# Performance work log

Measured on AMD Instinct MI355X. Metric: run time of the kernel, lower is better.

The kernel has to match this reference:

```python
import jax, jax.numpy as jnp
import numpy as np

B, P, K, KS = 512, 64, 30, 4      # graphs, nodes per graph, sort-pool k, conv1d kernel
N, E, F, H = B * P, 524288, 128, 256
N_CLASSES = 10
L_OUT = K - KS + 1                 # 27, conv1d output length


def _sage(h, wl, wr, b, src, dst, inv_deg):
    # PyG SAGEConv (mean aggr): out = lin_l(mean_j x_j) + lin_r(x_i); bias only on lin_l
    agg = jax.ops.segment_sum(h[src], dst, num_segments=N) * inv_deg
    return jax.nn.relu(agg @ wl + b + h @ wr)


def setup_inputs() -> dict:
    key = jax.random.key(0)
    ks = jax.random.split(key, 32)
    x = jax.random.normal(ks[0], (N, F), jnp.float32)
    # intra-graph random edges (src -> dst aggregation)
    g = jax.random.randint(ks[1], (E,), 0, B)
    src = g * P + jax.random.randint(ks[2], (E,), 0, P)
    dst = g * P + jax.random.randint(ks[3], (E,), 0, P)
    edge_index = jnp.stack([src, dst]).astype(jnp.int32)
    batch = jnp.repeat(jnp.arange(B), P).astype(jnp.int32)  # sorted graph ids

    def lin(k, i, o):
        return jax.random.normal(k, (i, o), jnp.float32) / np.float32(np.sqrt(i))

    inp = {"x": x, "edge_index": edge_index, "batch": batch}
    dims = [(F, H), (H, H), (H, H), (H, H)]
    ki = 4
    for li, (i, o) in enumerate(dims):
        inp[f"sage{li}_wl"] = lin(ks[ki], i, o); ki += 1
        inp[f"sage{li}_wr"] = lin(ks[ki], i, o); ki += 1
        inp[f"sage{li}_b"] = jnp.zeros((o,), jnp.float32)
    inp["conv1d_w"] = jax.random.normal(ks[ki], (H, H, KS), jnp.float32) / np.float32(np.sqrt(H * KS)); ki += 1
    inp["conv1d_b"] = jnp.zeros((H,), jnp.float32)
    inp["lin1_w"] = lin(ks[ki], H * L_OUT, H); ki += 1
    inp["lin1_b"] = jnp.zeros((H,), jnp.float32)
    inp["lin2_w"] = lin(ks[ki], H, 128); ki += 1
    inp["lin2_b"] = jnp.zeros((128,), jnp.float32)
    inp["out_w"] = lin(ks[ki], 128, N_CLASSES); ki += 1
    inp["out_b"] = jnp.zeros((N_CLASSES,), jnp.float32)
    return inp


def reference(x, edge_index, batch,
              sage0_wl, sage0_wr, sage0_b,
              sage1_wl, sage1_wr, sage1_b,
              sage2_wl, sage2_wr, sage2_b,
              sage3_wl, sage3_wr, sage3_b,
              conv1d_w, conv1d_b, lin1_w, lin1_b,
              lin2_w, lin2_b, out_w, out_b):
    src, dst = edge_index[0], edge_index[1]
    deg = jax.ops.segment_sum(jnp.ones(src.shape, x.dtype), dst, num_segments=N)
    inv_deg = (1.0 / jnp.maximum(deg, 1.0))[:, None]

    h = jnp.nan_to_num(x, nan=0.0)
    h = _sage(h, sage0_wl, sage0_wr, sage0_b, src, dst, inv_deg)
    h = _sage(h, sage1_wl, sage1_wr, sage1_b, src, dst, inv_deg)
    h = _sage(h, sage2_wl, sage2_wr, sage2_b, src, dst, inv_deg)
    h = _sage(h, sage3_wl, sage3_wr, sage3_b, src, dst, inv_deg)  # [N, H]

    # SortAggregation(k=K): to dense batch, sort by last channel desc, top-k, zero-pad
    counts = jax.ops.segment_sum(jnp.ones(N, jnp.int32), batch, num_segments=B)
    offsets = jnp.cumsum(counts) - counts
    pos = jnp.arange(N) - offsets[batch]
    D = h.shape[1]
    dense = jnp.zeros((B, P, D), h.dtype).at[batch, pos].set(h)
    valid = jnp.zeros((B, P), bool).at[batch, pos].set(True)
    skey = jnp.where(valid, dense[..., -1], -jnp.inf)
    order = jnp.argsort(-skey, axis=1)[:, :K]                       # [B, K]
    topk = jnp.take_along_axis(dense, order[..., None], axis=1)     # [B, K, D]
    tvalid = jnp.take_along_axis(valid, order, axis=1)
    topk = jnp.where(tvalid[..., None], topk, 0.0)

    # x.view(B, K, -1).permute(0, 2, 1) -> [B, D, K]
    xc = topk.transpose(0, 2, 1)
    y = jax.lax.conv_general_dilated(xc, conv1d_w, (1,), 'VALID',
                                     dimension_numbers=('NCH', 'OIH', 'NCH'))
    y = jax.nn.relu(y + conv1d_b[None, :, None])                    # [B, H, L_OUT]
    y = y.reshape(B, -1)                                            # dropout is identity in eval
    y = jax.nn.relu(y @ lin1_w + lin1_b)
    y = jax.nn.relu(y @ lin2_w + lin2_b)
    return jax.nn.relu(y @ out_w + out_b)                           # [B, N_CLASSES]
```

## Files before the change

kernel.cpp:

```cpp
#include <hip/hip_runtime.h>
#include <hip/hip_bf16.h>

#define NNODES 32768
#define NEDGES 524288
#define NGRAPH 512
#define PNODES 64
#define KTOP 30
#define FIN 128
#define HID 256
#define LOUT 27

#define C1F 4.8828125e-4f
#define C2F 2.384185791015625e-7f

using f16x8 = __attribute__((ext_vector_type(8))) _Float16;
using f16x4 = __attribute__((ext_vector_type(4))) _Float16;
using f32x4 = __attribute__((ext_vector_type(4))) float;
using f32x16 = __attribute__((ext_vector_type(16))) float;
using u32x4 = __attribute__((ext_vector_type(4))) uint32_t;

template<int N> struct IC { static constexpr int v = N; };

#define GLDS(src, dst) __builtin_amdgcn_global_load_lds( \
    (const __attribute__((address_space(1))) void*)(src), \
    (__attribute__((address_space(3))) void*)(dst), 16, 0, 0)

__global__ void hist_kernel(const int* __restrict__ dst, int* __restrict__ counts) {
    int e = blockIdx.x * blockDim.x + threadIdx.x;
    if (e < NEDGES) atomicAdd(&counts[dst[e]], 1);
}

__global__ __launch_bounds__(1024) void scan_block_kernel(const int* __restrict__ counts,
        int* __restrict__ loc, int* __restrict__ partial) {
    int b = blockIdx.x, t = threadIdx.x;
    int i = b * 1024 + t;
    int v = counts[i];
    int lane = t & 63, w = t >> 6;
    int x = v;
    #pragma unroll
    for (int d = 1; d < 64; d <<= 1) { int y = __shfl_up(x, d, 64); if (lane >= d) x += y; }
    __shared__ int ws[16];
    if (lane == 63) ws[w] = x;
    __syncthreads();
    if (w == 0) {
        int s = (lane < 16) ? ws[lane] : 0;
        #pragma unroll
        for (int d = 1; d < 16; d <<= 1) { int y = __shfl_up(s, d, 64); if (lane >= d) s += y; }
        if (lane < 16) ws[lane] = s;
    }
    __syncthreads();
    int base = (w > 0) ? ws[w - 1] : 0;
    int incl = base + x;
    loc[i] = incl - v;
    if (t == 1023) partial[b] = incl;
}

__global__ __launch_bounds__(1024) void scan_fixup_kernel(const int* __restrict__ loc,
        const int* __restrict__ partial, const int* __restrict__ counts,
        int* __restrict__ offsets, int* __restrict__ cursor, float* __restrict__ invdeg) {
    int b = blockIdx.x, t = threadIdx.x;
    int i = b * 1024 + t;
    __shared__ int sbase;
    if (t == 0) { int s = 0; for (int j = 0; j < b; ++j) s += partial[j]; sbase = s; }
    __syncthreads();
    int o = loc[i] + sbase;
    offsets[i] = o;
    cursor[i] = o;
    invdeg[i] = 1.0f / fmaxf((float)counts[i], 1.0f);
}

__global__ void scatter_kernel(const int* __restrict__ src, const int* __restrict__ dst,
        int* __restrict__ cursor, int* __restrict__ ssrc) {
    int e = blockIdx.x * blockDim.x + threadIdx.x;
    if (e < NEDGES) {
        int d = dst[e];
        int p = atomicAdd(&cursor[d], 1);
        ssrc[p] = ((d & 63) << 6) | (src[e] & 63);
    }
}

__global__ void nan2num_split_kernel(const float* __restrict__ x,
        _Float16* __restrict__ oh, _Float16* __restrict__ ol, int n4) {
    int i = blockIdx.x * blockDim.x + threadIdx.x;
    if (i >= n4) return;
    float4 v = *(const float4*)(x + i * 4);
    float xs[4] = {v.x, v.y, v.z, v.w};
    f16x4 hh, ll;
    #pragma unroll
    for (int q = 0; q < 4; ++q) {
        float a = xs[q];
        a = (a != a) ? 0.f : a;
        _Float16 h = (_Float16)a;
        hh[q] = h;
        ll[q] = (_Float16)((a - (float)h) * 2048.0f);
    }
    *(f16x4*)(oh + (size_t)i * 4) = hh;
    *(f16x4*)(ol + (size_t)i * 4) = ll;
}

struct PrepSage {
    const float* src[8];
    _Float16* dh[8];
    _Float16* dl[8];
    int logK[8];
    int part[8];
};

__global__ __launch_bounds__(256) void prep_sage_kernel(PrepSage p) {
    int y = blockIdx.y;
    int idx = blockIdx.x * 256 + threadIdx.x;
    int lk = p.logK[y], K = 1 << lk;
    if (idx >= 256 * K) return;
    int n = idx >> lk, k = idx & (K - 1);
    float w = p.src[y][(size_t)k * 256 + n];
    _Float16 h = (_Float16)w;
    int wv = n >> 5, l31 = n & 31;
    int c = k >> 5, h2 = (k >> 4) & 1, hb = (k >> 3) & 1, j = k & 7;
    int NCH = K >> 5;
    size_t dst = (size_t)(wv * 2 + p.part[y]) * (size_t)(NCH * 1024)
               + (size_t)(c * 2 + h2) * 512 + (size_t)(hb * 32 + l31) * 8 + j;
    p.dh[y][dst] = h;
    p.dl[y][dst] = (_Float16)((w - (float)h) * 2048.0f);
}

__global__ __launch_bounds__(256) void prep_conv_kernel(const float* __restrict__ W,
        _Float16* __restrict__ b0, _Float16* __restrict__ b1) {
    int idx = blockIdx.x * 256 + threadIdx.x;
    int o = idx >> 10, k = idx & 1023;
    float w = W[(size_t)o * 1024 + (k & 255) * 4 + (k >> 8)];
    _Float16 h = (_Float16)w;
    b0[(size_t)o * 1024 + k] = h;
    b1[(size_t)o * 1024 + k] = (_Float16)((w - (float)h) * 2048.0f);
}

__global__ __launch_bounds__(256) void prep_lin1_kernel(const float* __restrict__ l1w,
        _Float16* __restrict__ wh, _Float16* __restrict__ wl_) {
    __shared__ float sh[64][65];
    int kb = blockIdx.x * 64;
    int nb = blockIdx.y * 64;
    int t = threadIdx.x;
    {
        int kk = t >> 2;
        int nc = (t & 3) * 16;
        int k = kb + kk, l = k >> 8, c = k & 255;
        const float* srow = l1w + (size_t)(c * 27 + l) * 256 + nb + nc;
        #pragma unroll
        for (int j = 0; j < 16; j += 4) {
            float4 v = *(const float4*)(srow + j);
            sh[kk][nc + j + 0] = v.x;
            sh[kk][nc + j + 1] = v.y;
            sh[kk][nc + j + 2] = v.z;
            sh[kk][nc + j + 3] = v.w;
        }
    }
    __syncthreads();
    {
        int nn = t >> 2;
        int kc = (t & 3) * 16;
        f16x8 oh[2], ol[2];
        #pragma unroll
        for (int j = 0; j < 16; ++j) {
            float x = sh[kc + j][nn];
            _Float16 h = (_Float16)x;
            oh[j >> 3][j & 7] = h;
            ol[j >> 3][j & 7] = (_Float16)((x - (float)h) * 2048.0f);
        }
        size_t o = (size_t)(nb + nn) * 6912 + kb + kc;
        *(f16x8*)(wh + o) = oh[0];
        *(f16x8*)(wh + o + 8) = oh[1];
        *(f16x8*)(wl_ + o) = ol[0];
        *(f16x8*)(wl_ + o + 8) = ol[1];
    }
}

struct SageWAll {
    const _Float16* wh[4];
    const _Float16* wl[4];
    const float* bias[4];
};

__global__ __launch_bounds__(512, 2) void fused_sage_all_kernel(
        const _Float16* __restrict__ hh, const _Float16* __restrict__ hl,
        const int* __restrict__ offsets, const int* __restrict__ counts,
        const int* __restrict__ ssrc, const float* __restrict__ invdeg,
        SageWAll W,
        _Float16* __restrict__ outh, _Float16* __restrict__ outl) {
    __shared__ __align__(16) _Float16 hp[2][8 * 2048];
    __shared__ __align__(16) uint32_t Sw[4096];
    const int g = blockIdx.x, t = threadIdx.x;
    const int lane = t & 63, wave = t >> 6;
    const int l31 = lane & 31, hb = lane >> 5;

    #pragma unroll
    for (int i = 0; i < 8; ++i) Sw[t + i * 512] = 0;

    {
        int a = lane >> 2, b = lane & 3;
        #pragma unroll
        for (int u0 = 0; u0 < 4; ++u0) {
            int u = u0 * 8 + wave;
            int part = u & 1;
            int cs = u >> 1;
            int c = cs >> 2, stripe = cs & 3;
            int row = stripe * 16 + a;
            int o = b ^ ((row >> 1) & 3) ^ (c & 3);
            const _Float16* src = (part ? hl : hh) + (size_t)g * (64 * FIN)
                                + (size_t)row * FIN + c * 32 + o * 8;
            GLDS(src, &hp[part][c * 2048 + stripe * 512]);
        }
    }
    const int gbeg = offsets[g * 64];
    const int gend = offsets[g * 64 + 63] + counts[g * 64 + 63];
    __syncthreads();

    for (int e = gbeg + t; e < gend; e += 512)
        atomicAdd(&Sw[ssrc[e] & 4095], 1u);
    __syncthreads();

    {
        int d = t >> 3, o = t & 7;
        float idg = invdeg[g * 64 + d];
        float v[8];
        #pragma unroll
        for (int j = 0; j < 8; ++j) v[j] = (float)Sw[(d << 6) + (o << 3) + j] * idg;
        __syncthreads();
        _Float16* Sp = (_Float16*)Sw;
        f16x8 s0, s1;
        #pragma unroll
        for (int j = 0; j < 8; ++j) {
            _Float16 h1 = (_Float16)v[j];
            s0[j] = h1;
            s1[j] = (_Float16)((v[j] - (float)h1) * 2048.0f);
        }
        int addr = (d << 6) + ((o ^ (d & 7)) << 3);
        *(f16x8*)&Sp[addr] = s0;
        *(f16x8*)&Sp[4096 + addr] = s1;
    }
    __syncthreads();

    const int col = (wave << 5) + l31;

    auto gemmKV = [&](auto NC, const _Float16* __restrict__ Bh,
                      const _Float16* __restrict__ Bl,
                      f32x16& a00, f32x16& a01, f32x16& a10, f32x16& a11) {
        constexpr int NCH = decltype(NC)::v;
        #pragma unroll 2
        for (int c = 0; c < NCH; ++c) {
            #pragma unroll
            for (int h2 = 0; h2 < 2; ++h2) {
                int slot = (2 * h2 + hb) ^ ((l31 >> 1) & 3) ^ (c & 3);
                int addr = c * 2048 + (l31 << 5) + (slot << 3);
                f16x8 ah0 = *(const f16x8*)&hp[0][addr];
                f16x8 al0 = *(const f16x8*)&hp[1][addr];
                f16x8 ah1 = *(const f16x8*)&hp[0][addr + 1024];
                f16x8 al1 = *(const f16x8*)&hp[1][addr + 1024];
                int ko = ((c << 1) + h2) * 512 + (lane << 3);
                f16x8 bh = *(const f16x8*)(Bh + ko);
                f16x8 bl = *(const f16x8*)(Bl + ko);
                a00 = __builtin_amdgcn_mfma_f32_32x32x16_f16(ah0, bh, a00, 0, 0, 0);
                a10 = __builtin_amdgcn_mfma_f32_32x32x16_f16(al0, bh, a10, 0, 0, 0);
                a10 = __builtin_amdgcn_mfma_f32_32x32x16_f16(ah0, bl, a10, 0, 0, 0);
                a01 = __builtin_amdgcn_mfma_f32_32x32x16_f16(ah1, bh, a01, 0, 0, 0);
                a11 = __builtin_amdgcn_mfma_f32_32x32x16_f16(al1, bh, a11, 0, 0, 0);
                a11 = __builtin_amdgcn_mfma_f32_32x32x16_f16(ah1, bl, a11, 0, 0, 0);
            }
        }
    };

    auto packpair = [](float x, float y, uint32_t& hw, uint32_t& lw) {
        _Float16 xh = (_Float16)x, yh = (_Float16)y;
        _Float16 xl = (_Float16)((x - (float)xh) * 2048.0f);
        _Float16 yl = (_Float16)((y - (float)yh) * 2048.0f);
        hw = (uint32_t)__builtin_bit_cast(unsigned short, xh)
           | ((uint32_t)__builtin_bit_cast(unsigned short, yh) << 16);
        lw = (uint32_t)__builtin_bit_cast(unsigned short, xl)
           | ((uint32_t)__builtin_bit_cast(unsigned short, yl) << 16);
    };

    auto spass = [&](int soffBase, const f32x16& pf0, const f32x16& pf1, f32x16& qf) {
        const _Float16* Sp = (const _Float16*)Sw;
        f32x16 sA = 0.f, sB = 0.f;
        #pragma unroll
        for (int kc = 0; kc < 4; ++kc) {
            const f32x16& pfk = (kc < 2) ? pf0 : pf1;
            const int i0 = ((2 * kc) & 3) * 4, i1 = ((2 * kc + 1) & 3) * 4;
            float kv0 = hb ? pfk[i1 + 0] : pfk[i0 + 0];
            float kv1 = hb ? pfk[i1 + 1] : pfk[i0 + 1];
            float kv2 = hb ? pfk[i1 + 2] : pfk[i0 + 2];
            float kv3 = hb ? pfk[i1 + 3] : pfk[i0 + 3];
            float sv0 = hb ? pfk[i0 + 0] : pfk[i1 + 0];
            float sv1 = hb ? pfk[i0 + 1] : pfk[i1 + 1];
            float sv2 = hb ? pfk[i0 + 2] : pfk[i1 + 2];
            float sv3 = hb ? pfk[i0 + 3] : pfk[i1 + 3];
            uint32_t kh0, kl0, kh1, kl1, sh0, sl0, sh1, sl1;
            packpair(kv0, kv1, kh0, kl0);
            packpair(kv2, kv3, kh1, kl1);
            packpair(sv0, sv1, sh0, sl0);
            packpair(sv2, sv3, sh1, sl1);
            uint32_t rh0 = (uint32_t)__shfl_xor((int)sh0, 32, 64);
            uint32_t rh1 = (uint32_t)__shfl_xor((int)sh1, 32, 64);
            uint32_t rl0 = (uint32_t)__shfl_xor((int)sl0, 32, 64);
            uint32_t rl1 = (uint32_t)__shfl_xor((int)sl1, 32, 64);
            u32x4 bhu, blu;
            bhu[0] = hb ? rh0 : kh0;  bhu[1] = hb ? rh1 : kh1;
            bhu[2] = hb ? kh0 : rh0;  bhu[3] = hb ? kh1 : rh1;
            blu[0] = hb ? rl0 : kl0;  blu[1] = hb ? rl1 : kl1;
            blu[2] = hb ? kl0 : rl0;  blu[3] = hb ? kl1 : rl1;
            f16x8 bhv = __builtin_bit_cast(f16x8, bhu);
            f16x8 blv = __builtin_bit_cast(f16x8, blu);
            int soff = soffBase + (l31 << 6) + (((2 * kc + hb) ^ (l31 & 7)) << 3);
            f16x8 s0a = *(const f16x8*)&Sp[soff];
            f16x8 s1a = *(const f16x8*)&Sp[4096 + soff];
            sA = __builtin_amdgcn_mfma_f32_32x32x16_f16(s0a, bhv, sA, 0, 0, 0);
            sB = __builtin_amdgcn_mfma_f32_32x32x16_f16(s0a, blv, sB, 0, 0, 0);
            sB = __builtin_amdgcn_mfma_f32_32x32x16_f16(s1a, bhv, sB, 0, 0, 0);
        }
        qf += sA + C1F * sB;
    };

    auto run_layer = [&](auto NC, const _Float16* __restrict__ Wsh,
                         const _Float16* __restrict__ Wsl,
                         const float* __restrict__ bias,
                         f32x16& sC0, f32x16& sC1) {
        constexpr size_t wstride = (size_t)decltype(NC)::v * 1024;
        f32x16 q00 = 0.f, q01 = 0.f, q10 = 0.f, q11 = 0.f;
        gemmKV(NC, Wsh + (size_t)((wave << 1) + 1) * wstride,
               Wsl + (size_t)((wave << 1) + 1) * wstride, q00, q01, q10, q11);
        f32x16 qf0 = q00 + C1F * q10;
        f32x16 qf1 = q01 + C1F * q11;

        f32x16 p00 = 0.f, p01 = 0.f, p10 = 0.f, p11 = 0.f;
        gemmKV(NC, Wsh + (size_t)(wave << 1) * wstride,
               Wsl + (size_t)(wave << 1) * wstride, p00, p01, p10, p11);
        f32x16 pf0 = p00 + C1F * p10;
        f32x16 pf1 = p01 + C1F * p11;

        spass(0, pf0, pf1, qf0);
        spass(2048, pf0, pf1, qf1);

        const float bb = bias[col];
        #pragma unroll
        for (int reg = 0; reg < 16; ++reg) {
            sC0[reg] = fmaxf(qf0[reg] + bb, 0.f);
            sC1[reg] = fmaxf(qf1[reg] + bb, 0.f);
        }
    };

    auto hp_write = [&](const f32x16& sC0, const f32x16& sC1) {
        int oc = l31 >> 3, j = l31 & 7;
        #pragma unroll
        for (int mi = 0; mi < 2; ++mi)
            #pragma unroll
            for (int reg = 0; reg < 16; ++reg) {
                int row = (mi << 5) + (reg & 3) + ((reg >> 2) << 3) + (hb << 2);
                int slot = oc ^ ((row >> 1) & 3) ^ (wave & 3);
                int addr = wave * 2048 + (row << 5) + (slot << 3) + j;
                float v = mi ? sC1[reg] : sC0[reg];
                _Float16 h1 = (_Float16)v;
                hp[0][addr] = h1;
                hp[1][addr] = (_Float16)((v - (float)h1) * 2048.0f);
            }
    };

    f32x16 sC0, sC1;
    run_layer(IC<4>{}, W.wh[0], W.wl[0], W.bias[0], sC0, sC1);
    __syncthreads();
    hp_write(sC0, sC1);
    __syncthreads();
    run_layer(IC<8>{}, W.wh[1], W.wl[1], W.bias[1], sC0, sC1);
    __syncthreads();
    hp_write(sC0, sC1);
    __syncthreads();
    run_layer(IC<8>{}, W.wh[2], W.wl[2], W.bias[2], sC0, sC1);
    __syncthreads();
    hp_write(sC0, sC1);
    __syncthreads();
    run_layer(IC<8>{}, W.wh[3], W.wl[3], W.bias[3], sC0, sC1);
    __syncthreads();
    _Float16* eL = &hp[0][0];
    #pragma unroll
    for (int part = 0; part < 2; ++part) {
        #pragma unroll
        for (int mi = 0; mi < 2; ++mi) {
            #pragma unroll
            for (int reg = 0; reg < 16; ++reg) {
                int row = (mi << 5) + (reg & 3) + ((reg >> 2) << 3) + (hb << 2);
                int cx = col ^ ((((row >> 2) & 1) << 5) | ((row & 3) << 3));
                float v = mi ? sC1[reg] : sC0[reg];
                _Float16 h1 = (_Float16)v;
                eL[(row << 8) + cx] = part ? (_Float16)((v - (float)h1) * 2048.0f) : h1;
            }
        }
        __syncthreads();
        _Float16* gout = part ? outl : outh;
        #pragma unroll
        for (int it = 0; it < 4; ++it) {
            int i = (t << 3) + (it << 12);
            int row = i >> 8, cc = i & 255;
            int sx = cc ^ ((((row >> 2) & 1) << 5) | ((row & 3) << 3));
            f16x8 v8 = *(const f16x8*)&eL[(row << 8) + sx];
            *(f16x8*)(gout + (size_t)((g << 6) + row) * HID + cc) = v8;
        }
        if (part == 0) __syncthreads();
    }
}

template<int NPROD, int CONV, int NPAIRS, int EPI>
__global__ __launch_bounds__(256, 2) void mfma_ps_kernel(
        const _Float16* __restrict__ A1h, const _Float16* __restrict__ A1l,
        const _Float16* __restrict__ A2h, const _Float16* __restrict__ A2l,
        const _Float16* __restrict__ B1h, const _Float16* __restrict__ B1l,
        const _Float16* __restrict__ B2h, const _Float16* __restrict__ B2l,
        const float* __restrict__ bias,
        _Float16* __restrict__ outh, _Float16* __restrict__ outl,
        float* __restrict__ Cpart,
        int lda, int K, int Nd, int nrb) {
    __shared__ _Float16 As[2][2][128 * 32];
    __shared__ _Float16 Bs[2][2][128 * 32];
    const int t = threadIdx.x;
    const int lane = t & 63, wave = t >> 6;
    const int wr = wave & 1, wc = wave >> 1;
    const int bid = blockIdx.x;
    const int rb = bid % nrb, cb = bid / nrb;
    const int row0 = rb * 128, col0 = cb * 128;
    const int l31 = lane & 31, hb = lane >> 5, x3 = l31 & 3;
    const int r16 = lane >> 2;
    const int qsrc8 = ((lane & 3) ^ (r16 & 3)) * 8;
    size_t aoffj[2], boffj[2];
    #pragma unroll
    for (int j = 0; j < 2; ++j) {
        int ar = row0 + wave * 32 + j * 16 + r16;
        aoffj[j] = CONV ? ((size_t)ar * 256 + (size_t)(ar / 27) * 768)
                        : (size_t)ar * (size_t)lda;
        boffj[j] = (size_t)(col0 + wave * 32 + j * 16 + r16) * (size_t)K;
    }
    int aroff[2], broff[2], slot8[2];
    #pragma unroll
    for (int mi = 0; mi < 2; ++mi) aroff[mi] = (wr * 64 + mi * 32 + l31) * 32;
    #pragma unroll
    for (int ni = 0; ni < 2; ++ni) broff[ni] = (wc * 64 + ni * 32 + l31) * 32;
    #pragma unroll
    for (int h = 0; h < 2; ++h) slot8[h] = ((2 * h + hb) ^ x3) * 8;

    const int KV = NPAIRS * K;
    const int kchunk = KV / gridDim.z;
    const int kv_lo = blockIdx.z * kchunk, kv_hi = kv_lo + kchunk;

    f32x16 acc0[2][2], acc1[2][2], acc2[2][2];
    #pragma unroll
    for (int i = 0; i < 2; ++i)
        #pragma unroll
        for (int j = 0; j < 2; ++j) { acc0[i][j] = 0.f; acc1[i][j] = 0.f; acc2[i][j] = 0.f; }

    auto stage = [&](int kv, int b) {
        int p = (NPAIRS == 2 && kv >= K) ? 1 : 0;
        int k = kv - p * K;
        const _Float16* __restrict__ sAh = p ? A2h : A1h;
        const _Float16* __restrict__ sAl = p ? A2l : A1l;
        const _Float16* __restrict__ sBh = p ? B2h : B1h;
        const _Float16* __restrict__ sBl = p ? B2l : B1l;
        #pragma unroll
        for (int j = 0; j < 2; ++j) {
            int ldsbase = (wave * 32 + j * 16) * 32;
            size_t ga = aoffj[j] + k + qsrc8;
            size_t gb = boffj[j] + k + qsrc8;
            GLDS(sAh + ga, &As[b][0][ldsbase]);
            GLDS(sAl + ga, &As[b][1][ldsbase]);
            GLDS(sBh + gb, &Bs[b][0][ldsbase]);
            GLDS(sBl + gb, &Bs[b][1][ldsbase]);
        }
    };

    stage(kv_lo, 0);
    __syncthreads();
    int b = 0;
    for (int kv = kv_lo; kv < kv_hi; kv += 32) {
        if (kv + 32 < kv_hi) stage(kv + 32, b ^ 1);
        #pragma unroll
        for (int h = 0; h < 2; ++h) {
            f16x8 af0[2], af1[2], bf0[2], bf1[2];
            #pragma unroll
            for (int mi = 0; mi < 2; ++mi) {
                af0[mi] = *(const f16x8*)&As[b][0][aroff[mi] + slot8[h]];
                af1[mi] = *(const f16x8*)&As[b][1][aroff[mi] + slot8[h]];
            }
            #pragma unroll
            for (int ni = 0; ni < 2; ++ni) {
                bf0[ni] = *(const f16x8*)&Bs[b][0][broff[ni] + slot8[h]];
                bf1[ni] = *(const f16x8*)&Bs[b][1][broff[ni] + slot8[h]];
            }
            #pragma unroll
            for (int mi = 0; mi < 2; ++mi)
                #pragma unroll
                for (int ni = 0; ni < 2; ++ni) {
                    acc0[mi][ni] = __builtin_amdgcn_mfma_f32_32x32x16_f16(af0[mi], bf0[ni], acc0[mi][ni], 0, 0, 0);
                    acc1[mi][ni] = __builtin_amdgcn_mfma_f32_32x32x16_f16(af1[mi], bf0[ni], acc1[mi][ni], 0, 0, 0);
                    acc1[mi][ni] = __builtin_amdgcn_mfma_f32_32x32x16_f16(af0[mi], bf1[ni], acc1[mi][ni], 0, 0, 0);
                    if (NPROD == 4)
                        acc2[mi][ni] = __builtin_amdgcn_mfma_f32_32x32x16_f16(af1[mi], bf1[ni], acc2[mi][ni], 0, 0, 0);
                }
        }
        b ^= 1;
        __syncthreads();
    }

    const int rquad = 4 * hb;
    #pragma unroll
    for (int ni = 0; ni < 2; ++ni) {
        int col = col0 + wc * 64 + ni * 32 + l31;
        float bb = (EPI == 0) ? bias[col] : 0.f;
        #pragma unroll
        for (int mi = 0; mi < 2; ++mi) {
            #pragma unroll
            for (int reg = 0; reg < 16; ++reg) {
                float v = acc0[mi][ni][reg] + C1F * acc1[mi][ni][reg];
                if (NPROD == 4) v += C2F * acc2[mi][ni][reg];
                int row = row0 + wr * 64 + mi * 32 + (reg & 3) + 8 * (reg >> 2) + rquad;
                if (EPI == 0) {
                    v = fmaxf(v + bb, 0.f);
                    _Float16 h = (_Float16)v;
                    size_t o = (size_t)row * Nd + col;
                    outh[o] = h;
                    outl[o] = (_Float16)((v - (float)h) * 2048.0f);
                } else {
                    size_t zb = (size_t)blockIdx.z * (size_t)(nrb * 128) * Nd;
                    Cpart[zb + (size_t)row * Nd + col] = v;
                }
            }
        }
    }
}

__global__ __launch_bounds__(256) void sortgather_kernel(const _Float16* __restrict__ hh,
        const _Float16* __restrict__ hl, _Float16* __restrict__ th, _Float16* __restrict__ tl) {
    __shared__ float vals[PNODES];
    __shared__ int ord[KTOP];
    int g = blockIdx.x, t = threadIdx.x;
    if (t < PNODES) {
        size_t idx = (size_t)(g * PNODES + t) * HID + (HID - 1);
        vals[t] = (float)hh[idx] + C1F * (float)hl[idx];
    }
    __syncthreads();
    if (t < PNODES) {
        float v = vals[t];
        int rank = 0;
        for (int j = 0; j < PNODES; ++j) {
            float vj = vals[j];
            rank += (vj > v) || (vj == v && j < t);
        }
        if (rank < KTOP) ord[rank] = g * PNODES + t;
    }
    __syncthreads();
    int c8 = (t & 31) * 8;
    for (int r = t >> 5; r < KTOP; r += 8) {
        size_t s = (size_t)ord[r] * HID + c8;
        size_t d = (size_t)(g * KTOP + r) * HID + c8;
        *(f16x8*)(th + d) = *(const f16x8*)(hh + s);
        *(f16x8*)(tl + d) = *(const f16x8*)(hl + s);
    }
}

__global__ void reduce_conv_kernel(const float* __restrict__ yb32,
        const float* __restrict__ b, _Float16* __restrict__ ybh, _Float16* __restrict__ ybl) {
    int i = blockIdx.x * 256 + threadIdx.x;
    float v = fmaxf(yb32[i] + yb32[i + 13824 * 256] + b[i & 255], 0.f);
    _Float16 h = (_Float16)v;
    ybh[i] = h;
    ybl[i] = (_Float16)((v - (float)h) * 2048.0f);
}

__global__ void reduce_lin1_kernel(const float* __restrict__ z1p,
        const float* __restrict__ b, float* __restrict__ z1) {
    int i = blockIdx.x * 256 + threadIdx.x;
    float s = b[i & 255];
    #pragma unroll
    for (int z = 0; z < 27; ++z) s += z1p[(size_t)z * 131072 + i];
    z1[i] = fmaxf(s, 0.f);
}

__global__ __launch_bounds__(256) void gemm64_kernel(
        const float* __restrict__ A, const float* __restrict__ B,
        const float* __restrict__ bias, float* __restrict__ C,
        int lda, int kend, int Nd) {
    __shared__ float As[16][64];
    __shared__ float Bs[16][64];
    const int tid = threadIdx.x;
    const int tx = tid & 15, ty = tid >> 4;
    const int la_r = tid >> 2, la_c = (tid & 3) << 2;
    const int lb_r = tid >> 4, lb_c = (tid & 15) << 2;
    const int row0 = blockIdx.x * 64, col0 = blockIdx.y * 64;
    const size_t aoff = (size_t)(row0 + la_r) * (size_t)lda;
    float acc[4][4] = {};
    for (int k0 = 0; k0 < kend; k0 += 16) {
        __syncthreads();
        float4 av = *(const float4*)(A + aoff + k0 + la_c);
        As[la_c + 0][la_r] = av.x;
        As[la_c + 1][la_r] = av.y;
        As[la_c + 2][la_r] = av.z;
        As[la_c + 3][la_r] = av.w;
        *(float4*)&Bs[lb_r][lb_c] = *(const float4*)(B + (size_t)(k0 + lb_r) * Nd + col0 + lb_c);
        __syncthreads();
        #pragma unroll
        for (int k = 0; k < 16; ++k) {
            float4 a = *(const float4*)&As[k][ty << 2];
            float4 b = *(const float4*)&Bs[k][tx << 2];
            acc[0][0] += a.x * b.x; acc[0][1] += a.x * b.y; acc[0][2] += a.x * b.z; acc[0][3] += a.x * b.w;
            acc[1][0] += a.y * b.x; acc[1][1] += a.y * b.y; acc[1][2] += a.y * b.z; acc[1][3] += a.y * b.w;
            acc[2][0] += a.z * b.x; acc[2][1] += a.z * b.y; acc[2][2] += a.z * b.z; acc[2][3] += a.z * b.w;
            acc[3][0] += a.w * b.x; acc[3][1] += a.w * b.y; acc[3][2] += a.w * b.z; acc[3][3] += a.w * b.w;
        }
    }
    #pragma unroll
    for (int i = 0; i < 4; ++i) {
        int row = row0 + (ty << 2) + i;
        #pragma unroll
        for (int j = 0; j < 4; ++j) {
            int col = col0 + (tx << 2) + j;
            C[(size_t)row * Nd + col] = fmaxf(acc[i][j] + bias[col], 0.f);
        }
    }
}

__global__ void out_kernel(const float* __restrict__ z2, const float* __restrict__ w,
        const float* __restrict__ b, float* __restrict__ out) {
    int idx = blockIdx.x * blockDim.x + threadIdx.x;
    if (idx < NGRAPH * 10) {
        int r = idx / 10, c = idx % 10;
        float s = b[c];
        for (int k = 0; k < 128; ++k) s += z2[r * 128 + k] * w[k * 10 + c];
        out[idx] = fmaxf(s, 0.f);
    }
}

extern "C" void kernel_launch(void* const* d_in, const int* in_sizes, int n_in,
                              void* d_out, int out_size, void* d_ws, size_t ws_size,
                              hipStream_t stream) {
    const float* x    = (const float*)d_in[0];
    const int*   edge = (const int*)d_in[1];
    const int*   esrc = edge;
    const int*   edst = edge + NEDGES;
    const float* wl[4] = {(const float*)d_in[3], (const float*)d_in[6], (const float*)d_in[9],  (const float*)d_in[12]};
    const float* wr[4] = {(const float*)d_in[4], (const float*)d_in[7], (const float*)d_in[10], (const float*)d_in[13]};
    const float* sb[4] = {(const float*)d_in[5], (const float*)d_in[8], (const float*)d_in[11], (const float*)d_in[14]};
    const float* convw = (const float*)d_in[15];
    const float* convb = (const float*)d_in[16];
    const float* l1w   = (const float*)d_in[17];
    const float* l1b   = (const float*)d_in[18];
    const float* l2w   = (const float*)d_in[19];
    const float* l2b   = (const float*)d_in[20];
    const float* ow    = (const float*)d_in[21];
    const float* ob    = (const float*)d_in[22];
    float* out = (float*)d_out;

    char* ws = (char*)d_ws;
    size_t off = 0;
    auto alloc = [&](size_t bytes) -> char* {
        char* p = ws + off;
        off = (off + bytes + 255) & ~(size_t)255;
        return p;
    };
    int*   counts  = (int*)alloc((size_t)NNODES * 4);
    int*   offsets = (int*)alloc((size_t)NNODES * 4);
    int*   cursor  = (int*)alloc((size_t)NNODES * 4);
    int*   loc     = (int*)alloc((size_t)NNODES * 4);
    int*   partial = (int*)alloc(32 * 4);
    float* invdeg  = (float*)alloc((size_t)NNODES * 4);
    int*   ssrc    = (int*)alloc((size_t)NEDGES * 4);
    _Float16* wch[4]; _Float16* wcl[4];
    for (int l = 0; l < 4; ++l) {
        size_t kb = (size_t)512 * (l ? HID : FIN) * 2;
        wch[l] = (_Float16*)alloc(kb);
        wcl[l] = (_Float16*)alloc(kb);
    }
    _Float16* cvh = (_Float16*)alloc((size_t)HID * 1024 * 2);
    _Float16* cvl = (_Float16*)alloc((size_t)HID * 1024 * 2);

    const size_t H0T = (size_t)NNODES * FIN * 2;
    const size_t AGT = (size_t)NNODES * HID * 2;
    const size_t TKT = (size_t)NGRAPH * KTOP * HID * 2;
    const size_t YBT = (size_t)NGRAPH * LOUT * HID * 2;
    const size_t YB32T = (size_t)2 * 13824 * 256 * 4;
    const size_t W1T = (size_t)HID * 6912 * 2;

    char* R1 = alloc(2 * H0T);
    char* R2 = alloc(2 * AGT);
    char* R3 = alloc(2 * AGT);
    char* R4 = alloc(2 * AGT);
    _Float16* h0h = (_Float16*)R1; _Float16* h0l = (_Float16*)(R1 + H0T);
    _Float16* tkh = (_Float16*)R1; _Float16* tkl = (_Float16*)(R1 + TKT);
    _Float16* ybh = (_Float16*)R2; _Float16* ybl_ = (_Float16*)(R2 + YBT);
    float* yb32 = (float*)(R2 + 2 * YBT);
    float* z1p  = (float*)(R2 + 2 * YBT);
    char* tail2 = R2 + 2 * YBT + YB32T;
    float* z1  = (float*)tail2;
    float* z2  = (float*)(tail2 + (size_t)NGRAPH * HID * 4);
    _Float16* w1h = (_Float16*)(tail2 + (size_t)NGRAPH * HID * 4 + (size_t)NGRAPH * 128 * 4 + 256);
    _Float16* w1l = (_Float16*)((char*)w1h + W1T);
    _Float16* hBh = (_Float16*)R4; _Float16* hBl = (_Float16*)(R4 + AGT);

    hipMemsetAsync(counts, 0, (size_t)NNODES * 4, stream);
    hist_kernel<<<NEDGES / 256, 256, 0, stream>>>(edst, counts);
    scan_block_kernel<<<NNODES / 1024, 1024, 0, stream>>>(counts, loc, partial);
    scan_fixup_kernel<<<NNODES / 1024, 1024, 0, stream>>>(loc, partial, counts, offsets, cursor, invdeg);
    scatter_kernel<<<NEDGES / 256, 256, 0, stream>>>(esrc, edst, cursor, ssrc);
    nan2num_split_kernel<<<(NNODES * FIN / 4) / 256, 256, 0, stream>>>(x, h0h, h0l, NNODES * FIN / 4);

    PrepSage ps;
    for (int l = 0; l < 4; ++l) {
        int lk = l ? 8 : 7;
        ps.src[2 * l] = wl[l];     ps.dh[2 * l] = wch[l];     ps.dl[2 * l] = wcl[l];
        ps.src[2 * l + 1] = wr[l]; ps.dh[2 * l + 1] = wch[l]; ps.dl[2 * l + 1] = wcl[l];
        ps.logK[2 * l] = lk;     ps.part[2 * l] = 0;
        ps.logK[2 * l + 1] = lk; ps.part[2 * l + 1] = 1;
    }
    prep_sage_kernel<<<dim3(256, 8), 256, 0, stream>>>(ps);
    prep_conv_kernel<<<(HID * 1024) / 256, 256, 0, stream>>>(convw, cvh, cvl);

    SageWAll swa;
    for (int l = 0; l < 4; ++l) { swa.wh[l] = wch[l]; swa.wl[l] = wcl[l]; swa.bias[l] = sb[l]; }
    fused_sage_all_kernel<<<NGRAPH, 512, 0, stream>>>(
        h0h, h0l, offsets, counts, ssrc, invdeg, swa, hBh, hBl);

    sortgather_kernel<<<NGRAPH, 256, 0, stream>>>(hBh, hBl, tkh, tkl);
    prep_lin1_kernel<<<dim3(108, 4), 256, 0, stream>>>(l1w, w1h, w1l);

    mfma_ps_kernel<3, 1, 1, 1><<<dim3(108 * 2, 1, 2), 256, 0, stream>>>(
        tkh, tkl, nullptr, nullptr, cvh, cvl, nullptr, nullptr, nullptr, nullptr, nullptr, yb32, 256, 1024, HID, 108);
    reduce_conv_kernel<<<13824 * 256 / 256, 256, 0, stream>>>(yb32, convb, ybh, ybl_);

    mfma_ps_kernel<3, 0, 1, 1><<<dim3(4 * 2, 1, 27), 256, 0, stream>>>(
        ybh, ybl_, nullptr, nullptr, w1h, w1l, nullptr, nullptr, nullptr, nullptr, nullptr, z1p, 6912, 6912, HID, 4);
    reduce_lin1_kernel<<<NGRAPH * HID / 256, 256, 0, stream>>>(z1p, l1b, z1);

    gemm64_kernel<<<dim3(NGRAPH / 64, 128 / 64), 256, 0, stream>>>(z1, l2w, l2b, z2, HID, HID, 128);

    out_kernel<<<(NGRAPH * 10 + 255) / 256, 256, 0, stream>>>(z2, ow, ob, out);
}
```

Baseline: 433.0 us.

## Fuse prep kernels, fold sort-pool into SAGE kernel, restructure MFMA loop

Merges the four weight and input conversion kernels into one launch that branches on block index. Moves the sort-pool top-k selection and gather into the tail of the fused SAGE kernel, so the full per-node output no longer goes to global memory and is not read back. Reworks the inner GEMM into per-row-half passes with software-prefetched B fragments, which halves the live accumulators per call but reads the B operands twice. The main risks are extra register pressure from full unrolling and a longer serial tail in the SAGE kernel.

```diff
diff --git a/kernel.cpp b/kernel.cpp
--- a/kernel.cpp
+++ b/kernel.cpp
@@ -79,25 +79,6 @@
     }
 }
 
-__global__ void nan2num_split_kernel(const float* __restrict__ x,
-        _Float16* __restrict__ oh, _Float16* __restrict__ ol, int n4) {
-    int i = blockIdx.x * blockDim.x + threadIdx.x;
-    if (i >= n4) return;
-    float4 v = *(const float4*)(x + i * 4);
-    float xs[4] = {v.x, v.y, v.z, v.w};
-    f16x4 hh, ll;
-    #pragma unroll
-    for (int q = 0; q < 4; ++q) {
-        float a = xs[q];
-        a = (a != a) ? 0.f : a;
-        _Float16 h = (_Float16)a;
-        hh[q] = h;
-        ll[q] = (_Float16)((a - (float)h) * 2048.0f);
-    }
-    *(f16x4*)(oh + (size_t)i * 4) = hh;
-    *(f16x4*)(ol + (size_t)i * 4) = ll;
-}
-
 struct PrepSage {
     const float* src[8];
     _Float16* dh[8];
@@ -106,70 +87,92 @@
     int part[8];
 };
 
-__global__ __launch_bounds__(256) void prep_sage_kernel(PrepSage p) {
-    int y = blockIdx.y;
-    int idx = blockIdx.x * 256 + threadIdx.x;
-    int lk = p.logK[y], K = 1 << lk;
-    if (idx >= 256 * K) return;
-    int n = idx >> lk, k = idx & (K - 1);
-    float w = p.src[y][(size_t)k * 256 + n];
-    _Float16 h = (_Float16)w;
-    int wv = n >> 5, l31 = n & 31;
-    int c = k >> 5, h2 = (k >> 4) & 1, hb = (k >> 3) & 1, j = k & 7;
-    int NCH = K >> 5;
-    size_t dst = (size_t)(wv * 2 + p.part[y]) * (size_t)(NCH * 1024)
-               + (size_t)(c * 2 + h2) * 512 + (size_t)(hb * 32 + l31) * 8 + j;
-    p.dh[y][dst] = h;
-    p.dl[y][dst] = (_Float16)((w - (float)h) * 2048.0f);
-}
-
-__global__ __launch_bounds__(256) void prep_conv_kernel(const float* __restrict__ W,
-        _Float16* __restrict__ b0, _Float16* __restrict__ b1) {
-    int idx = blockIdx.x * 256 + threadIdx.x;
-    int o = idx >> 10, k = idx & 1023;
-    float w = W[(size_t)o * 1024 + (k & 255) * 4 + (k >> 8)];
-    _Float16 h = (_Float16)w;
-    b0[(size_t)o * 1024 + k] = h;
-    b1[(size_t)o * 1024 + k] = (_Float16)((w - (float)h) * 2048.0f);
-}
-
-__global__ __launch_bounds__(256) void prep_lin1_kernel(const float* __restrict__ l1w,
-        _Float16* __restrict__ wh, _Float16* __restrict__ wl_) {
+struct PrepAll {
+    const float* x;
+    _Float16* h0h; _Float16* h0l;
+    PrepSage ps;
+    const float* convw; _Float16* cvh; _Float16* cvl;
+    const float* l1w; _Float16* w1h; _Float16* w1l;
+};
+
+__global__ __launch_bounds__(256) void prep_all_kernel(PrepAll P) {
     __shared__ float sh[64][65];
-    int kb = blockIdx.x * 64;
-    int nb = blockIdx.y * 64;
-    int t = threadIdx.x;
-    {
-        int kk = t >> 2;
-        int nc = (t & 3) * 16;
-        int k = kb + kk, l = k >> 8, c = k & 255;
-        const float* srow = l1w + (size_t)(c * 27 + l) * 256 + nb + nc;
-        #pragma unroll
-        for (int j = 0; j < 16; j += 4) {
-            float4 v = *(const float4*)(srow + j);
-            sh[kk][nc + j + 0] = v.x;
-            sh[kk][nc + j + 1] = v.y;
-            sh[kk][nc + j + 2] = v.z;
-            sh[kk][nc + j + 3] = v.w;
-        }
-    }
-    __syncthreads();
-    {
-        int nn = t >> 2;
-        int kc = (t & 3) * 16;
-        f16x8 oh[2], ol[2];
-        #pragma unroll
-        for (int j = 0; j < 16; ++j) {
-            float x = sh[kc + j][nn];
-            _Float16 h = (_Float16)x;
-            oh[j >> 3][j & 7] = h;
-            ol[j >> 3][j & 7] = (_Float16)((x - (float)h) * 2048.0f);
-        }
-        size_t o = (size_t)(nb + nn) * 6912 + kb + kc;
-        *(f16x8*)(wh + o) = oh[0];
-        *(f16x8*)(wh + o + 8) = oh[1];
-        *(f16x8*)(wl_ + o) = ol[0];
-        *(f16x8*)(wl_ + o + 8) = ol[1];
+    const int b = blockIdx.x, t = threadIdx.x;
+    if (b < 4096) {
+        int i = b * 256 + t;
+        float4 v = *(const float4*)(P.x + (size_t)i * 4);
+        float xs[4] = {v.x, v.y, v.z, v.w};
+        f16x4 hh, ll;
+        #pragma unroll
+        for (int q = 0; q < 4; ++q) {
+            float a = xs[q];
+            a = (a != a) ? 0.f : a;
+            _Float16 h = (_Float16)a;
+            hh[q] = h;
+            ll[q] = (_Float16)((a - (float)h) * 2048.0f);
+        }
+        *(f16x4*)(P.h0h + (size_t)i * 4) = hh;
+        *(f16x4*)(P.h0l + (size_t)i * 4) = ll;
+    } else if (b < 6144) {
+        int seg = b - 4096;
+        int y = seg >> 8;
+        int idx = (seg & 255) * 256 + t;
+        int lk = P.ps.logK[y], K = 1 << lk;
+        if (idx < 256 * K) {
+            int n = idx >> lk, k = idx & (K - 1);
+            float w = P.ps.src[y][(size_t)k * 256 + n];
+            _Float16 h = (_Float16)w;
+            int wv = n >> 5, l31 = n & 31;
+            int c = k >> 5, h2 = (k >> 4) & 1, hb = (k >> 3) & 1, j = k & 7;
+            int NCH = K >> 5;
+            size_t dst = (size_t)(wv * 2 + P.ps.part[y]) * (size_t)(NCH * 1024)
+                       + (size_t)(c * 2 + h2) * 512 + (size_t)(hb * 32 + l31) * 8 + j;
+            P.ps.dh[y][dst] = h;
+            P.ps.dl[y][dst] = (_Float16)((w - (float)h) * 2048.0f);
+        }
+    } else if (b < 7168) {
+        int idx = (b - 6144) * 256 + t;
+        int o = idx >> 10, k = idx & 1023;
+        float w = P.convw[(size_t)o * 1024 + (k & 255) * 4 + (k >> 8)];
+        _Float16 h = (_Float16)w;
+        P.cvh[(size_t)o * 1024 + k] = h;
+        P.cvl[(size_t)o * 1024 + k] = (_Float16)((w - (float)h) * 2048.0f);
+    } else {
+        int seg = b - 7168;
+        int kb = (seg % 108) * 64;
+        int nb = (seg / 108) * 64;
+        {
+            int kk = t >> 2;
+            int nc = (t & 3) * 16;
+            int k = kb + kk, l = k >> 8, c = k & 255;
+            const float* srow = P.l1w + (size_t)(c * 27 + l) * 256 + nb + nc;
+            #pragma unroll
+            for (int j = 0; j < 16; j += 4) {
+                float4 v = *(const float4*)(srow + j);
+                sh[kk][nc + j + 0] = v.x;
+                sh[kk][nc + j + 1] = v.y;
+                sh[kk][nc + j + 2] = v.z;
+                sh[kk][nc + j + 3] = v.w;
+            }
+        }
+        __syncthreads();
+        {
+            int nn = t >> 2;
+            int kc = (t & 3) * 16;
+            f16x8 oh[2], ol[2];
+            #pragma unroll
+            for (int j = 0; j < 16; ++j) {
+                float x = sh[kc + j][nn];
+                _Float16 h = (_Float16)x;
+                oh[j >> 3][j & 7] = h;
+                ol[j >> 3][j & 7] = (_Float16)((x - (float)h) * 2048.0f);
+            }
+            size_t o = (size_t)(nb + nn) * 6912 + kb + kc;
+            *(f16x8*)(P.w1h + o) = oh[0];
+            *(f16x8*)(P.w1h + o + 8) = oh[1];
+            *(f16x8*)(P.w1l + o) = ol[0];
+            *(f16x8*)(P.w1l + o + 8) = ol[1];
+        }
     }
 }
 
@@ -184,7 +187,7 @@
         const int* __restrict__ offsets, const int* __restrict__ counts,
         const int* __restrict__ ssrc, const float* __restrict__ invdeg,
         SageWAll W,
-        _Float16* __restrict__ outh, _Float16* __restrict__ outl) {
+        _Float16* __restrict__ tkh, _Float16* __restrict__ tkl) {
     __shared__ __align__(16) _Float16 hp[2][8 * 2048];
     __shared__ __align__(16) uint32_t Sw[4096];
     const int g = blockIdx.x, t = threadIdx.x;
@@ -240,31 +243,30 @@
 
     const int col = (wave << 5) + l31;
 
-    auto gemmKV = [&](auto NC, const _Float16* __restrict__ Bh,
-                      const _Float16* __restrict__ Bl,
-                      f32x16& a00, f32x16& a01, f32x16& a10, f32x16& a11) {
-        constexpr int NCH = decltype(NC)::v;
-        #pragma unroll 2
-        for (int c = 0; c < NCH; ++c) {
-            #pragma unroll
-            for (int h2 = 0; h2 < 2; ++h2) {
-                int slot = (2 * h2 + hb) ^ ((l31 >> 1) & 3) ^ (c & 3);
-                int addr = c * 2048 + (l31 << 5) + (slot << 3);
-                f16x8 ah0 = *(const f16x8*)&hp[0][addr];
-                f16x8 al0 = *(const f16x8*)&hp[1][addr];
-                f16x8 ah1 = *(const f16x8*)&hp[0][addr + 1024];
-                f16x8 al1 = *(const f16x8*)&hp[1][addr + 1024];
-                int ko = ((c << 1) + h2) * 512 + (lane << 3);
-                f16x8 bh = *(const f16x8*)(Bh + ko);
-                f16x8 bl = *(const f16x8*)(Bl + ko);
-                a00 = __builtin_amdgcn_mfma_f32_32x32x16_f16(ah0, bh, a00, 0, 0, 0);
-                a10 = __builtin_amdgcn_mfma_f32_32x32x16_f16(al0, bh, a10, 0, 0, 0);
-                a10 = __builtin_amdgcn_mfma_f32_32x32x16_f16(ah0, bl, a10, 0, 0, 0);
-                a01 = __builtin_amdgcn_mfma_f32_32x32x16_f16(ah1, bh, a01, 0, 0, 0);
-                a11 = __builtin_amdgcn_mfma_f32_32x32x16_f16(al1, bh, a11, 0, 0, 0);
-                a11 = __builtin_amdgcn_mfma_f32_32x32x16_f16(ah1, bl, a11, 0, 0, 0);
+    auto gemmHalf = [&](auto NC, const _Float16* __restrict__ Bh,
+                        const _Float16* __restrict__ Bl, int rowOff) -> f32x16 {
+        constexpr int NIT = decltype(NC)::v * 2;
+        const int lo8 = lane << 3;
+        f32x16 a0 = 0.f, a1 = 0.f;
+        f16x8 bhN = *(const f16x8*)(Bh + lo8);
+        f16x8 blN = *(const f16x8*)(Bl + lo8);
+        #pragma unroll
+        for (int it = 0; it < NIT; ++it) {
+            const int c = it >> 1, h2 = it & 1;
+            f16x8 bh = bhN, bl = blN;
+            if (it + 1 < NIT) {
+                bhN = *(const f16x8*)(Bh + (it + 1) * 512 + lo8);
+                blN = *(const f16x8*)(Bl + (it + 1) * 512 + lo8);
             }
-        }
+            const int slot = (2 * h2 + hb) ^ ((l31 >> 1) & 3) ^ (c & 3);
+            const int addr = rowOff + c * 2048 + (l31 << 5) + (slot << 3);
+            f16x8 ah = *(const f16x8*)&hp[0][addr];
+            f16x8 al = *(const f16x8*)&hp[1][addr];
+            a0 = __builtin_amdgcn_mfma_f32_32x32x16_f16(ah, bh, a0, 0, 0, 0);
+            a1 = __builtin_amdgcn_mfma_f32_32x32x16_f16(al, bh, a1, 0, 0, 0);
+            a1 = __builtin_amdgcn_mfma_f32_32x32x16_f16(ah, bl, a1, 0, 0, 0);
+        }
+        return a0 + C1F * a1;
     };
 
     auto packpair = [](float x, float y, uint32_t& hw, uint32_t& lw) {
@@ -323,21 +325,16 @@
                          const float* __restrict__ bias,
                          f32x16& sC0, f32x16& sC1) {
         constexpr size_t wstride = (size_t)decltype(NC)::v * 1024;
-        f32x16 q00 = 0.f, q01 = 0.f, q10 = 0.f, q11 = 0.f;
-        gemmKV(NC, Wsh + (size_t)((wave << 1) + 1) * wstride,
-               Wsl + (size_t)((wave << 1) + 1) * wstride, q00, q01, q10, q11);
-        f32x16 qf0 = q00 + C1F * q10;
-        f32x16 qf1 = q01 + C1F * q11;
-
-        f32x16 p00 = 0.f, p01 = 0.f, p10 = 0.f, p11 = 0.f;
-        gemmKV(NC, Wsh + (size_t)(wave << 1) * wstride,
-               Wsl + (size_t)(wave << 1) * wstride, p00, p01, p10, p11);
-        f32x16 pf0 = p00 + C1F * p10;
-        f32x16 pf1 = p01 + C1F * p11;
-
+        const _Float16* BqH = Wsh + (size_t)((wave << 1) + 1) * wstride;
+        const _Float16* BqL = Wsl + (size_t)((wave << 1) + 1) * wstride;
+        const _Float16* BpH = Wsh + (size_t)(wave << 1) * wstride;
+        const _Float16* BpL = Wsl + (size_t)(wave << 1) * wstride;
+        f32x16 qf0 = gemmHalf(NC, BqH, BqL, 0);
+        f32x16 qf1 = gemmHalf(NC, BqH, BqL, 1024);
+        f32x16 pf0 = gemmHalf(NC, BpH, BpL, 0);
+        f32x16 pf1 = gemmHalf(NC, BpH, BpL, 1024);
         spass(0, pf0, pf1, qf0);
         spass(2048, pf0, pf1, qf1);
-
         const float bb = bias[col];
         #pragma unroll
         for (int reg = 0; reg < 16; ++reg) {
@@ -377,31 +374,45 @@
     __syncthreads();
     run_layer(IC<8>{}, W.wh[3], W.wl[3], W.bias[3], sC0, sC1);
     __syncthreads();
-    _Float16* eL = &hp[0][0];
-    #pragma unroll
-    for (int part = 0; part < 2; ++part) {
-        #pragma unroll
-        for (int mi = 0; mi < 2; ++mi) {
-            #pragma unroll
-            for (int reg = 0; reg < 16; ++reg) {
-                int row = (mi << 5) + (reg & 3) + ((reg >> 2) << 3) + (hb << 2);
-                int cx = col ^ ((((row >> 2) & 1) << 5) | ((row & 3) << 3));
-                float v = mi ? sC1[reg] : sC0[reg];
-                _Float16 h1 = (_Float16)v;
-                eL[(row << 8) + cx] = part ? (_Float16)((v - (float)h1) * 2048.0f) : h1;
-            }
-        }
-        __syncthreads();
-        _Float16* gout = part ? outl : outh;
-        #pragma unroll
-        for (int it = 0; it < 4; ++it) {
-            int i = (t << 3) + (it << 12);
-            int row = i >> 8, cc = i & 255;
-            int sx = cc ^ ((((row >> 2) & 1) << 5) | ((row & 3) << 3));
-            f16x8 v8 = *(const f16x8*)&eL[(row << 8) + sx];
-            *(f16x8*)(gout + (size_t)((g << 6) + row) * HID + cc) = v8;
-        }
-        if (part == 0) __syncthreads();
+
+    #pragma unroll
+    for (int mi = 0; mi < 2; ++mi) {
+        #pragma unroll
+        for (int reg = 0; reg < 16; ++reg) {
+            int row = (mi << 5) + (reg & 3) + ((reg >> 2) << 3) + (hb << 2);
+            int cx = col ^ ((((row >> 2) & 1) << 5) | ((row & 3) << 3));
+            float v = mi ? sC1[reg] : sC0[reg];
+            _Float16 h1 = (_Float16)v;
+            hp[0][(row << 8) + cx] = h1;
+            hp[1][(row << 8) + cx] = (_Float16)((v - (float)h1) * 2048.0f);
+        }
+    }
+    __syncthreads();
+
+    float* vals = (float*)Sw;
+    int* ords = (int*)(Sw + 64);
+    if (t < 64) {
+        int sx = 255 ^ ((((t >> 2) & 1) << 5) | ((t & 3) << 3));
+        vals[t] = (float)hp[0][(t << 8) + sx] + C1F * (float)hp[1][(t << 8) + sx];
+    }
+    __syncthreads();
+    if (t < 64) {
+        float v = vals[t];
+        int rank = 0;
+        for (int j = 0; j < 64; ++j) {
+            float vj = vals[j];
+            rank += (vj > v) || (vj == v && j < t);
+        }
+        if (rank < KTOP) ords[rank] = t;
+    }
+    __syncthreads();
+    for (int r = wave; r < KTOP; r += 8) {
+        int row = ords[r];
+        int cc = (lane & 31) << 3;
+        int sx = cc ^ ((((row >> 2) & 1) << 5) | ((row & 3) << 3));
+        size_t d = (size_t)(g * KTOP + r) * HID + cc;
+        if (lane < 32) *(f16x8*)(tkh + d) = *(const f16x8*)&hp[0][(row << 8) + sx];
+        else           *(f16x8*)(tkl + d) = *(const f16x8*)&hp[1][(row << 8) + sx];
     }
 }
 
@@ -531,35 +542,6 @@
     }
 }
 
-__global__ __launch_bounds__(256) void sortgather_kernel(const _Float16* __restrict__ hh,
-        const _Float16* __restrict__ hl, _Float16* __restrict__ th, _Float16* __restrict__ tl) {
-    __shared__ float vals[PNODES];
-    __shared__ int ord[KTOP];
-    int g = blockIdx.x, t = threadIdx.x;
-    if (t < PNODES) {
-        size_t idx = (size_t)(g * PNODES + t) * HID + (HID - 1);
-        vals[t] = (float)hh[idx] + C1F * (float)hl[idx];
-    }
-    __syncthreads();
-    if (t < PNODES) {
-        float v = vals[t];
-        int rank = 0;
-        for (int j = 0; j < PNODES; ++j) {
-            float vj = vals[j];
-            rank += (vj > v) || (vj == v && j < t);
-        }
-        if (rank < KTOP) ord[rank] = g * PNODES + t;
-    }
-    __syncthreads();
-    int c8 = (t & 31) * 8;
-    for (int r = t >> 5; r < KTOP; r += 8) {
-        size_t s = (size_t)ord[r] * HID + c8;
-        size_t d = (size_t)(g * KTOP + r) * HID + c8;
-        *(f16x8*)(th + d) = *(const f16x8*)(hh + s);
-        *(f16x8*)(tl + d) = *(const f16x8*)(hl + s);
-    }
-}
-
 __global__ void reduce_conv_kernel(const float* __restrict__ yb32,
         const float* __restrict__ b, _Float16* __restrict__ ybh, _Float16* __restrict__ ybl) {
     int i = blockIdx.x * 256 + threadIdx.x;
@@ -687,7 +669,7 @@
     char* R3 = alloc(2 * AGT);
     char* R4 = alloc(2 * AGT);
     _Float16* h0h = (_Float16*)R1; _Float16* h0l = (_Float16*)(R1 + H0T);
-    _Float16* tkh = (_Float16*)R1; _Float16* tkl = (_Float16*)(R1 + TKT);
+    _Float16* tkh = (_Float16*)R4; _Float16* tkl = (_Float16*)(R4 + TKT);
     _Float16* ybh = (_Float16*)R2; _Float16* ybl_ = (_Float16*)(R2 + YBT);
     float* yb32 = (float*)(R2 + 2 * YBT);
     float* z1p  = (float*)(R2 + 2 * YBT);
@@ -696,33 +678,30 @@
     float* z2  = (float*)(tail2 + (size_t)NGRAPH * HID * 4);
     _Float16* w1h = (_Float16*)(tail2 + (size_t)NGRAPH * HID * 4 + (size_t)NGRAPH * 128 * 4 + 256);
     _Float16* w1l = (_Float16*)((char*)w1h + W1T);
-    _Float16* hBh = (_Float16*)R4; _Float16* hBl = (_Float16*)(R4 + AGT);
 
     hipMemsetAsync(counts, 0, (size_t)NNODES * 4, stream);
     hist_kernel<<<NEDGES / 256, 256, 0, stream>>>(edst, counts);
     scan_block_kernel<<<NNODES / 1024, 1024, 0, stream>>>(counts, loc, partial);
     scan_fixup_kernel<<<NNODES / 1024, 1024, 0, stream>>>(loc, partial, counts, offsets, cursor, invdeg);
     scatter_kernel<<<NEDGES / 256, 256, 0, stream>>>(esrc, edst, cursor, ssrc);
-    nan2num_split_kernel<<<(NNODES * FIN / 4) / 256, 256, 0, stream>>>(x, h0h, h0l, NNODES * FIN / 4);
-
-    PrepSage ps;
+
+    PrepAll pa;
+    pa.x = x; pa.h0h = h0h; pa.h0l = h0l;
     for (int l = 0; l < 4; ++l) {
         int lk = l ? 8 : 7;
-        ps.src[2 * l] = wl[l];     ps.dh[2 * l] = wch[l];     ps.dl[2 * l] = wcl[l];
-        ps.src[2 * l + 1] = wr[l]; ps.dh[2 * l + 1] = wch[l]; ps.dl[2 * l + 1] = wcl[l];
-        ps.logK[2 * l] = lk;     ps.part[2 * l] = 0;
-        ps.logK[2 * l + 1] = lk; ps.part[2 * l + 1] = 1;
-    }
-    prep_sage_kernel<<<dim3(256, 8), 256, 0, stream>>>(ps);
-    prep_conv_kernel<<<(HID * 1024) / 256, 256, 0, stream>>>(convw, cvh, cvl);
+        pa.ps.src[2 * l] = wl[l];     pa.ps.dh[2 * l] = wch[l];     pa.ps.dl[2 * l] = wcl[l];
+        pa.ps.src[2 * l + 1] = wr[l]; pa.ps.dh[2 * l + 1] = wch[l]; pa.ps.dl[2 * l + 1] = wcl[l];
+        pa.ps.logK[2 * l] = lk;     pa.ps.part[2 * l] = 0;
+        pa.ps.logK[2 * l + 1] = lk; pa.ps.part[2 * l + 1] = 1;
+    }
+    pa.convw = convw; pa.cvh = cvh; pa.cvl = cvl;
+    pa.l1w = l1w; pa.w1h = w1h; pa.w1l = w1l;
+    prep_all_kernel<<<7600, 256, 0, stream>>>(pa);
 
     SageWAll swa;
     for (int l = 0; l < 4; ++l) { swa.wh[l] = wch[l]; swa.wl[l] = wcl[l]; swa.bias[l] = sb[l]; }
     fused_sage_all_kernel<<<NGRAPH, 512, 0, stream>>>(
-        h0h, h0l, offsets, counts, ssrc, invdeg, swa, hBh, hBl);
-
-    sortgather_kernel<<<NGRAPH, 256, 0, stream>>>(hBh, hBl, tkh, tkl);
-    prep_lin1_kernel<<<dim3(108, 4), 256, 0, stream>>>(l1w, w1h, w1l);
+        h0h, h0l, offsets, counts, ssrc, invdeg, swa, tkh, tkl);
 
     mfma_ps_kernel<3, 1, 1, 1><<<dim3(108 * 2, 1, 2), 256, 0, stream>>>(
         tkh, tkl, nullptr, nullptr, cvh, cvl, nullptr, nullptr, nullptr, nullptr, nullptr, yb32, 256, 1024, HID, 108);
```

Result: no change. 433.2 us, median of 2 (+0.0%).
